# Kernel optimization log

Hardware: AMD Instinct MI355X
Metric: run time of the kernel (lower is better)

The kernel has to match this reference:

```python
import jax, jax.numpy as jnp
import numpy as np

FACTOR = 1.0
MARGIN = 0.5
NUM_CLASS = 19


def setup_inputs() -> dict:
    key = jax.random.key(0)
    k1, k2, k3 = jax.random.split(key, 3)
    B, C, H, W = 8, 256, 128, 128
    features = jax.random.normal(k1, (B, C, H, W), dtype=jnp.float32)
    labels = jax.random.randint(k2, (B, H, W), 0, NUM_CLASS, dtype=jnp.int32)
    prototypes = jax.random.normal(k3, (NUM_CLASS, C), dtype=jnp.float32)
    return {"features": features, "labels": labels, "prototypes": prototypes}


def reference(features, labels, prototypes):
    b, c, h, w = features.shape
    # flatten to [N, C] pixels and [N] labels (labels already at (h, w))
    feat = jnp.transpose(features, (0, 2, 3, 1)).reshape(-1, c)
    lab = labels.reshape(-1)
    # per-class mean via one-pass segment reduce (all classes present)
    sums = jax.ops.segment_sum(feat, lab, num_segments=NUM_CLASS)          # [K, C]
    counts = jax.ops.segment_sum(jnp.ones_like(lab, feat.dtype), lab,
                                 num_segments=NUM_CLASS)                   # [K]
    means = sums / jnp.maximum(counts, 1.0)[:, None]
    # L2 normalize (torch F.normalize uses eps=1e-12 clamp on the norm)
    norms = jnp.maximum(jnp.linalg.norm(means, axis=1, keepdims=True), 1e-12)
    mn = means / norms
    # pairwise cosine distance, diagonal forced to 2.0
    D = 1.0 - mn @ mn.T                                                    # [K, K]
    D = jnp.where(jnp.eye(NUM_CLASS, dtype=bool), 2.0, D)
    loss = jnp.mean(jnp.maximum(MARGIN - D, 0.0))
    return FACTOR * loss
```

## Files before the change

### kernel.cpp

```cpp
#include <hip/hip_runtime.h>
#include <hip/hip_bf16.h>

namespace {

constexpr int K  = 19;
constexpr int C  = 256;
constexpr int HW = 16384;
constexpr int B  = 8;

__global__ __launch_bounds__(256) void fsl_accum(const float* __restrict__ feat,
                                                 const int* __restrict__ labels,
                                                 float* __restrict__ sums) {
    __shared__ float acc[4][K][64];
    const int tid  = threadIdx.x;
    const int lane = tid & 63;
    const int w    = tid >> 6;
    const int c    = blockIdx.x;
    const int b    = blockIdx.y;

    for (int i = tid; i < 4 * K * 64; i += 256) ((float*)acc)[i] = 0.f;
    __syncthreads();

    const float* fp = feat + (size_t)(b * C + c) * HW;
    const int*   lp = labels + (size_t)b * HW;
    float* mya = &acc[w][0][lane];

    #pragma unroll 4
    for (int it = 0; it < HW / 1024; ++it) {
        const int px  = it * 1024 + tid * 4;
        const float4 v  = *(const float4*)(fp + px);
        const int4   lb = *(const int4*)(lp + px);
        mya[lb.x * 64] += v.x;
        mya[lb.y * 64] += v.y;
        mya[lb.z * 64] += v.z;
        mya[lb.w * 64] += v.w;
    }
    __syncthreads();

    for (int idx = tid; idx < K * 64; idx += 256) {
        const int k = idx >> 6, l = idx & 63;
        acc[0][k][l] = acc[0][k][l] + acc[1][k][l] + acc[2][k][l] + acc[3][k][l];
    }
    __syncthreads();

    for (int k = w; k < K; k += 4) {
        float v = acc[0][k][lane];
        v += __shfl_down(v, 32);
        v += __shfl_down(v, 16);
        v += __shfl_down(v, 8);
        v += __shfl_down(v, 4);
        v += __shfl_down(v, 2);
        v += __shfl_down(v, 1);
        if (lane == 0) atomicAdd(&sums[k * C + c], v);
    }
}

__global__ __launch_bounds__(256) void fsl_count(const int* __restrict__ labels,
                                                 float* __restrict__ counts) {
    __shared__ int cnt[K];
    const int tid = threadIdx.x;
    if (tid < K) cnt[tid] = 0;
    __syncthreads();

    const int* lp = labels + (size_t)blockIdx.x * 2048;
    #pragma unroll
    for (int it = 0; it < 2; ++it) {
        const int4 lb = *(const int4*)(lp + it * 1024 + tid * 4);
        atomicAdd(&cnt[lb.x], 1);
        atomicAdd(&cnt[lb.y], 1);
        atomicAdd(&cnt[lb.z], 1);
        atomicAdd(&cnt[lb.w], 1);
    }
    __syncthreads();
    if (tid < K) atomicAdd(&counts[tid], (float)cnt[tid]);
}

__global__ __launch_bounds__(384) void fsl_finalize(const float* __restrict__ sums,
                                                    const float* __restrict__ counts,
                                                    float* __restrict__ out) {
    __shared__ float mm[K][260];
    __shared__ float rcount[K];
    __shared__ float norm2s[K];
    __shared__ float rnorm[K];
    __shared__ float wred[6];
    const int tid = threadIdx.x;

    if (tid < K) rcount[tid] = 1.0f / fmaxf(counts[tid], 1.0f);
    __syncthreads();

    if (tid < C) {
        #pragma unroll
        for (int k = 0; k < K; ++k) mm[k][tid] = sums[k * C + tid] * rcount[k];
    }
    __syncthreads();

    if (tid < K * 16) {
        const int k = tid >> 4, sub = tid & 15;
        float s = 0.f;
        #pragma unroll
        for (int j = 0; j < 16; ++j) {
            const float v = mm[k][sub + j * 16];
            s += v * v;
        }
        s += __shfl_xor(s, 8);
        s += __shfl_xor(s, 4);
        s += __shfl_xor(s, 2);
        s += __shfl_xor(s, 1);
        if (sub == 0) norm2s[k] = s;
    }
    __syncthreads();
    if (tid < K) rnorm[tid] = 1.0f / fmaxf(sqrtf(norm2s[tid]), 1e-12f);
    __syncthreads();

    float contrib = 0.f;
    if (tid < K * K) {
        const int i = tid / K;
        const int j = tid - i * K;
        const float4* ri = (const float4*)&mm[i][0];
        const float4* rj = (const float4*)&mm[j][0];
        float dot = 0.f;
        #pragma unroll 8
        for (int q = 0; q < C / 4; ++q) {
            const float4 a = ri[q], bv = rj[q];
            dot += a.x * bv.x + a.y * bv.y + a.z * bv.z + a.w * bv.w;
        }
        const float g = dot * rnorm[i] * rnorm[j];
        contrib = (i == j) ? 0.f : fmaxf(g - 0.5f, 0.f);
    }

    float v = contrib;
    v += __shfl_down(v, 32);
    v += __shfl_down(v, 16);
    v += __shfl_down(v, 8);
    v += __shfl_down(v, 4);
    v += __shfl_down(v, 2);
    v += __shfl_down(v, 1);
    if ((tid & 63) == 0) wred[tid >> 6] = v;
    __syncthreads();
    if (tid == 0) {
        float t = 0.f;
        #pragma unroll
        for (int q = 0; q < 6; ++q) t += wred[q];
        out[0] = 1.0f * t / (float)(K * K);
    }
}

}

extern "C" void kernel_launch(void* const* d_in, const int* in_sizes, int n_in,
                              void* d_out, int out_size, void* d_ws, size_t ws_size,
                              hipStream_t stream) {
    const float* feat   = (const float*)d_in[0];
    const int*   labels = (const int*)d_in[1];

    float* sums   = (float*)d_ws;
    float* counts = sums + K * C;
    float* out    = (float*)d_out;

    hipMemsetAsync(d_ws, 0, (K * C + K) * sizeof(float), stream);

    dim3 gridA(C, B);
    fsl_accum<<<gridA, 256, 0, stream>>>(feat, labels, sums);
    fsl_count<<<64, 256, 0, stream>>>(labels, counts);
    fsl_finalize<<<1, 384, 0, stream>>>(sums, counts, out);
}
```

Baseline: 202.9 us.

## Fuse label counting into accumulation kernel and replace atomics with per-batch partials

Removes the separate count kernel by having the c==0 blocks of the accumulate kernel also histogram labels. Global float atomics on sums are replaced by per-batch partial writes, which lets the memset be dropped and moves the batch reduction into the finalize kernel. This saves two launches/dispatches and atomic contention, but adds LDS atomics to one block per batch, which could make those blocks stragglers.

```diff
diff --git a/kernel.cpp b/kernel.cpp
--- a/kernel.cpp
+++ b/kernel.cpp
@@ -10,15 +10,19 @@
 
 __global__ __launch_bounds__(256) void fsl_accum(const float* __restrict__ feat,
                                                  const int* __restrict__ labels,
-                                                 float* __restrict__ sums) {
+                                                 float* __restrict__ psums,
+                                                 float* __restrict__ pcounts) {
     __shared__ float acc[4][K][64];
+    __shared__ int   cnt[4][32];
     const int tid  = threadIdx.x;
     const int lane = tid & 63;
     const int w    = tid >> 6;
     const int c    = blockIdx.x;
     const int b    = blockIdx.y;
+    const bool do_count = (c == 0);
 
     for (int i = tid; i < 4 * K * 64; i += 256) ((float*)acc)[i] = 0.f;
+    if (tid < 128) ((int*)cnt)[tid] = 0;
     __syncthreads();
 
     const float* fp = feat + (size_t)(b * C + c) * HW;
@@ -34,6 +38,12 @@
         mya[lb.y * 64] += v.y;
         mya[lb.z * 64] += v.z;
         mya[lb.w * 64] += v.w;
+        if (do_count) {
+            atomicAdd(&cnt[w][lb.x], 1);
+            atomicAdd(&cnt[w][lb.y], 1);
+            atomicAdd(&cnt[w][lb.z], 1);
+            atomicAdd(&cnt[w][lb.w], 1);
+        }
     }
     __syncthreads();
 
@@ -51,32 +61,16 @@
         v += __shfl_down(v, 4);
         v += __shfl_down(v, 2);
         v += __shfl_down(v, 1);
-        if (lane == 0) atomicAdd(&sums[k * C + c], v);
+        if (lane == 0) psums[((size_t)b * K + k) * C + c] = v;
+    }
+    if (do_count && tid < K) {
+        pcounts[b * K + tid] =
+            (float)(cnt[0][tid] + cnt[1][tid] + cnt[2][tid] + cnt[3][tid]);
     }
 }
 
-__global__ __launch_bounds__(256) void fsl_count(const int* __restrict__ labels,
-                                                 float* __restrict__ counts) {
-    __shared__ int cnt[K];
-    const int tid = threadIdx.x;
-    if (tid < K) cnt[tid] = 0;
-    __syncthreads();
-
-    const int* lp = labels + (size_t)blockIdx.x * 2048;
-    #pragma unroll
-    for (int it = 0; it < 2; ++it) {
-        const int4 lb = *(const int4*)(lp + it * 1024 + tid * 4);
-        atomicAdd(&cnt[lb.x], 1);
-        atomicAdd(&cnt[lb.y], 1);
-        atomicAdd(&cnt[lb.z], 1);
-        atomicAdd(&cnt[lb.w], 1);
-    }
-    __syncthreads();
-    if (tid < K) atomicAdd(&counts[tid], (float)cnt[tid]);
-}
-
-__global__ __launch_bounds__(384) void fsl_finalize(const float* __restrict__ sums,
-                                                    const float* __restrict__ counts,
+__global__ __launch_bounds__(384) void fsl_finalize(const float* __restrict__ psums,
+                                                    const float* __restrict__ pcounts,
                                                     float* __restrict__ out) {
     __shared__ float mm[K][260];
     __shared__ float rcount[K];
@@ -85,12 +79,22 @@
     __shared__ float wred[6];
     const int tid = threadIdx.x;
 
-    if (tid < K) rcount[tid] = 1.0f / fmaxf(counts[tid], 1.0f);
+    if (tid < K) {
+        float cc = 0.f;
+        #pragma unroll
+        for (int b = 0; b < B; ++b) cc += pcounts[b * K + tid];
+        rcount[tid] = 1.0f / fmaxf(cc, 1.0f);
+    }
     __syncthreads();
 
     if (tid < C) {
         #pragma unroll
-        for (int k = 0; k < K; ++k) mm[k][tid] = sums[k * C + tid] * rcount[k];
+        for (int k = 0; k < K; ++k) {
+            float s = 0.f;
+            #pragma unroll
+            for (int b = 0; b < B; ++b) s += psums[((size_t)b * K + k) * C + tid];
+            mm[k][tid] = s * rcount[k];
+        }
     }
     __syncthreads();
 
@@ -153,14 +157,11 @@
     const float* feat   = (const float*)d_in[0];
     const int*   labels = (const int*)d_in[1];
 
-    float* sums   = (float*)d_ws;
-    float* counts = sums + K * C;
-    float* out    = (float*)d_out;
-
-    hipMemsetAsync(d_ws, 0, (K * C + K) * sizeof(float), stream);
+    float* psums   = (float*)d_ws;
+    float* pcounts = psums + B * K * C;
+    float* out     = (float*)d_out;
 
     dim3 gridA(C, B);
-    fsl_accum<<<gridA, 256, 0, stream>>>(feat, labels, sums);
-    fsl_count<<<64, 256, 0, stream>>>(labels, counts);
-    fsl_finalize<<<1, 384, 0, stream>>>(sums, counts, out);
+    fsl_accum<<<gridA, 256, 0, stream>>>(feat, labels, psums, pcounts);
+    fsl_finalize<<<1, 384, 0, stream>>>(psums, pcounts, out);
 }
```

Result: no change. 200.5 us (-1.2%).
